# Kernel optimization log

Measured on AMD Instinct MI355X. Metric: run time of the kernel, lower is better.

## Reference

```python
import jax, jax.numpy as jnp
import numpy as np

HIDDEN = 768
ENT = 9
D = 64  # inner_dim
BIG = 1e12


def _rope_tables(seq_len, dim):
    # layout after torch stack([sin,cos],-1).reshape: [sin0,cos0,sin1,cos1,...]
    pos = jnp.arange(seq_len, dtype=jnp.float32)[:, None]          # [S,1]
    inv = jnp.power(10000.0, -2.0 * jnp.arange(dim // 2, dtype=jnp.float32) / dim)
    ang = pos * inv                                                 # [S,D/2]
    # repeat_interleave(2): [c0,c0,c1,c1,...]
    cos = jnp.repeat(jnp.cos(ang), 2, axis=-1)[:, None, :]          # [S,1,D]
    sin = jnp.repeat(jnp.sin(ang), 2, axis=-1)[:, None, :]
    return sin, cos


def _rotate_half_interleaved(x):
    # stack([-x_odd, x_even], -1).reshape -> [-x1, x0, -x3, x2, ...]
    return jnp.stack([-x[..., 1::2], x[..., ::2]], axis=-1).reshape(x.shape)


def _multilabel_ce(logits, labels):
    # standard GlobalPointer multilabel categorical crossentropy
    B = logits.shape[0]
    y_pred = logits.reshape(B * ENT, -1)
    y_true = labels.reshape(B * ENT, -1)
    y_pred = (1.0 - 2.0 * y_true) * y_pred
    y_neg = y_pred - y_true * BIG
    y_pos = y_pred - (1.0 - y_true) * BIG
    neg = jnp.logaddexp(0.0, jax.scipy.special.logsumexp(y_neg, axis=-1))
    pos = jnp.logaddexp(0.0, jax.scipy.special.logsumexp(y_pos, axis=-1))
    return jnp.mean(neg + pos)


def setup_inputs() -> dict:
    key = jax.random.key(0)
    k1, k2, k3, k4 = jax.random.split(key, 4)
    B, S = 16, 512
    last_hidden_state = jax.random.normal(k1, (B, S, HIDDEN), dtype=jnp.float32)
    attention_mask = jnp.ones((B, S), dtype=jnp.int32)
    batch_labels = jax.random.randint(k2, (B, ENT, S, S), 0, 2).astype(jnp.int32)
    W = jax.random.normal(k3, (HIDDEN, ENT * D * 2), dtype=jnp.float32) * 0.02
    b = jnp.zeros((ENT * D * 2,), dtype=jnp.float32)
    return {"last_hidden_state": last_hidden_state, "attention_mask": attention_mask,
            "batch_labels": batch_labels, "W": W, "b": b}


def reference(last_hidden_state, attention_mask, batch_labels, W, b):
    B, S, _ = last_hidden_state.shape
    out = last_hidden_state @ W + b                     # [B,S,ENT*2D]
    out = out.reshape(B, S, ENT, 2 * D)
    qw, kw = out[..., :D], out[..., D:]                 # [B,S,ENT,D]

    sin, cos = _rope_tables(S, D)                       # [S,1,D]
    qw = qw * cos + _rotate_half_interleaved(qw) * sin
    kw = kw * cos + _rotate_half_interleaved(kw) * sin

    logits = jnp.einsum('bmhd,bnhd->bhmn', qw, kw)      # [B,ENT,S,S]

    pad = attention_mask.astype(jnp.float32)[:, None, None, :]  # mask over key dim n
    logits = logits * pad - (1.0 - pad) * BIG
    tril = jnp.tril(jnp.ones((S, S), dtype=jnp.float32), -1)
    logits = logits - tril * BIG
    temp_logits = logits / (D ** 0.5)

    loss = _multilabel_ce(temp_logits, batch_labels.astype(jnp.float32))
    return loss, temp_logits
```

## Files before the change

kernel.cpp:

```cpp
#include <hip/hip_runtime.h>
#include <hip/hip_bf16.h>

#define HID 768
#define ENTS 9
#define DD 64
#define NOUT 1152
#define BATCH 16
#define SEQ 512
#define BIGF 1000000000000.0f
#define BIG8 125000000000.0f
#define NCHUNK 16

typedef __attribute__((ext_vector_type(8))) short short8;
typedef __attribute__((ext_vector_type(4))) short short4_t;
typedef __attribute__((ext_vector_type(4))) float floatx4;
typedef __attribute__((ext_vector_type(2))) float floatx2;
typedef __attribute__((ext_vector_type(4))) int intx4;
typedef unsigned short ushort_t;

static __device__ __forceinline__ ushort_t f2bf(float x) {
    unsigned int u = __float_as_uint(x);
    unsigned int r = (u + 0x7FFFu + ((u >> 16) & 1u)) >> 16;
    return (ushort_t)r;
}

static __device__ __forceinline__ void gload16(const void* g, void* l) {
    __builtin_amdgcn_global_load_lds(
        (const __attribute__((address_space(1))) void*)g,
        (__attribute__((address_space(3))) void*)l, 16, 0, 0);
}

__global__ __launch_bounds__(256) void prep_kernel(
    const float* __restrict__ X, const float* __restrict__ W,
    float* __restrict__ sin_t, float* __restrict__ cos_t,
    ushort_t* __restrict__ Xb, ushort_t* __restrict__ Wt)
{
    const int tid = blockIdx.x * 256 + threadIdx.x;
    const int nth = gridDim.x * 256;

    for (int idx = tid; idx < SEQ * 32; idx += nth) {
        int m = idx >> 5, i = idx & 31;
        float inv = powf(10000.0f, -2.0f * (float)i / 64.0f);
        float ang = (float)m * inv;
        sin_t[idx] = sinf(ang);
        cos_t[idx] = cosf(ang);
    }
    for (int idx = tid; idx < NOUT * HID; idx += nth) {
        int n = idx / HID, k = idx - n * HID;
        Wt[idx] = f2bf(W[(size_t)k * NOUT + n]);
    }
    const int nx4 = BATCH * SEQ * HID / 4;
    for (int idx = tid; idx < nx4; idx += nth) {
        float4 f = *(const float4*)&X[idx * 4];
        ushort_t* p = &Xb[idx * 4];
        p[0] = f2bf(f.x); p[1] = f2bf(f.y); p[2] = f2bf(f.z); p[3] = f2bf(f.w);
    }
}

__global__ __launch_bounds__(256) void proj_rope_kernel(
    const ushort_t* __restrict__ Xb, const ushort_t* __restrict__ Wt,
    const float* __restrict__ bias,
    const float* __restrict__ sin_t, const float* __restrict__ cos_t,
    ushort_t* __restrict__ qbuf, ushort_t* __restrict__ kbuf)
{
    __shared__ ushort_t As[128 * 32];
    __shared__ ushort_t Bs[128 * 32];
    const int tid  = threadIdx.x;
    const int lane = tid & 63;
    const int wave = tid >> 6;
    const int bm = blockIdx.x * 128;
    const int bn = blockIdx.y * 128;
    const int wm = (wave >> 1) * 64;
    const int wn = (wave & 1) * 64;

    floatx4 acc[4][4];
    #pragma unroll
    for (int j = 0; j < 4; ++j)
        #pragma unroll
        for (int i = 0; i < 4; ++i) { floatx4 z = {0.f,0.f,0.f,0.f}; acc[j][i] = z; }

    const int c0 = wave * 64 + lane;
    const int c1 = 256 + wave * 64 + lane;
    const int r0 = c0 >> 2, q0 = (c0 & 3) * 8;
    const int r1 = c1 >> 2, q1 = (c1 & 3) * 8;
    ushort_t* ldsA0 = As + wave * 512;
    ushort_t* ldsA1 = As + 2048 + wave * 512;
    ushort_t* ldsB0 = Bs + wave * 512;
    ushort_t* ldsB1 = Bs + 2048 + wave * 512;

    const int ko = (lane >> 4) * 8;
    const int lr = lane & 15;

    for (int kt = 0; kt < HID; kt += 32) {
        gload16(&Xb[(size_t)(bm + r0) * HID + kt + q0], ldsA0);
        gload16(&Xb[(size_t)(bm + r1) * HID + kt + q1], ldsA1);
        gload16(&Wt[(size_t)(bn + r0) * HID + kt + q0], ldsB0);
        gload16(&Wt[(size_t)(bn + r1) * HID + kt + q1], ldsB1);
        __syncthreads();

        short8 a[4], b[4];
        #pragma unroll
        for (int i = 0; i < 4; ++i) a[i] = *(const short8*)&As[(wm + i*16 + lr) * 32 + ko];
        #pragma unroll
        for (int j = 0; j < 4; ++j) b[j] = *(const short8*)&Bs[(wn + j*16 + lr) * 32 + ko];
        #pragma unroll
        for (int j = 0; j < 4; ++j)
            #pragma unroll
            for (int i = 0; i < 4; ++i)
                acc[j][i] = __builtin_amdgcn_mfma_f32_16x16x32_bf16(b[j], a[i], acc[j][i], 0, 0, 0);
        __syncthreads();
    }

    #pragma unroll
    for (int j = 0; j < 4; ++j) {
        const int n0 = bn + wn + j*16 + (lane >> 4) * 4;
        const int e   = n0 >> 7;
        const int dd0 = n0 & 127;
        const bool isq = dd0 < DD;
        const int d0  = isq ? dd0 : dd0 - DD;
        const float4 bv = *(const float4*)&bias[n0];
        #pragma unroll
        for (int i = 0; i < 4; ++i) {
            const int m = bm + wm + i*16 + lr;
            const int s  = m & (SEQ - 1);
            const int bb = m >> 9;
            const float c0f = cos_t[s*32 + (d0 >> 1)];
            const float s0f = sin_t[s*32 + (d0 >> 1)];
            const float c1f = cos_t[s*32 + (d0 >> 1) + 1];
            const float s1f = sin_t[s*32 + (d0 >> 1) + 1];
            const float v0 = acc[j][i][0] + bv.x;
            const float v1 = acc[j][i][1] + bv.y;
            const float v2 = acc[j][i][2] + bv.z;
            const float v3 = acc[j][i][3] + bv.w;
            const float o0 = v0 * c0f - v1 * s0f;
            const float o1 = v1 * c0f + v0 * s0f;
            const float o2 = v2 * c1f - v3 * s1f;
            const float o3 = v3 * c1f + v2 * s1f;
            short4_t sv = { (short)f2bf(o0), (short)f2bf(o1), (short)f2bf(o2), (short)f2bf(o3) };
            size_t oidx = (((size_t)(bb * ENTS + e) * SEQ) + s) * DD + d0;
            *(short4_t*)&(isq ? qbuf : kbuf)[oidx] = sv;
        }
    }
}

__global__ __launch_bounds__(256) void qk_mask_ce_kernel(
    const ushort_t* __restrict__ qbuf, const ushort_t* __restrict__ kbuf,
    const int* __restrict__ amask, const int* __restrict__ labels,
    float* __restrict__ logits, float* __restrict__ partials)
{
    __shared__ ushort_t Qs[128][72];
    __shared__ ushort_t Ks[128][72];
    __shared__ float ssn[4], ssp[4];
    const int tid  = threadIdx.x;
    const int xy = blockIdx.x;
    const int bh = blockIdx.y;
    const int bx = xy >> 2, by = xy & 3;
    const int bm = bx * 128;
    const int bn = by * 128;
    const int b  = bh / ENTS;
    const int bhbase = bh << 18;

    if (bx > by) {
        const int c4 = (tid & 31) << 2;
        const int rr = tid >> 5;

        const intx4 pf = *(const intx4*)&amask[(b << 9) + bn + c4];
        floatx4 cv;
        #pragma unroll
        for (int e = 0; e < 4; ++e) cv[e] = (float)pf[e] * BIG8 - 2.0f * BIG8;
        float cvm1 = 0.f;
        if (c4 > 0) {
            const int pfm1 = amask[(b << 9) + bn + c4 - 1];
            cvm1 = (float)pfm1 * BIG8 - 2.0f * BIG8;
        }
        const floatx4 sh = { cvm1, cv.x, cv.y, cv.z };
        const floatx2 h2 = { cv.y, cv.z };

        int cnt = 0;
        for (int pass = 0; pass < 16; ++pass) {
            const int m = bm + pass * 8 + rr;
            const int off = bhbase + (m << 9) + bn + c4;
            const intx4 y4 = __builtin_nontemporal_load((const intx4*)&labels[off]);
            #pragma unroll
            for (int e = 0; e < 4; ++e) cnt += (y4[e] & 1) & pf[e];
            if (c4 == 0) {
                logits[off] = cv.x;
                *(floatx2*)&logits[off + 1] = h2;
            } else {
                *(floatx4*)&logits[off - 1] = sh;
            }
            if (c4 == 124) logits[off + 3] = cv.w;
        }

        #pragma unroll
        for (int o = 32; o > 0; o >>= 1) cnt += __shfl_down(cnt, o);
        if ((tid & 63) == 0) ssn[tid >> 6] = (float)cnt;
        __syncthreads();
        if (tid == 0) {
            float SP = ssn[0] + ssn[1] + ssn[2] + ssn[3];
            floatx2 res = { 0.f, SP };
            *(floatx2*)&partials[(size_t)(bh * NCHUNK + xy) * 2] = res;
        }
        return;
    }

    const int lane = tid & 63;
    const int wave = tid >> 6;
    const int wm = (wave >> 1) * 64;
    const int wn = (wave & 1) * 64;
    const size_t base = (size_t)bh * SEQ * DD;

    const int g  = lane >> 4;
    const int lr = lane & 15;
    const int ko = g * 8;
    const int r0 = bm + wm + lr;
    const int W  = bn + wn;
    const int n00 = W + (g << 2);

    const bool diag = (bx == by);

    intx4 y[4][4];
    #pragma unroll
    for (int j = 0; j < 4; ++j)
        #pragma unroll
        for (int i = 0; i < 4; ++i)
            y[j][i] = __builtin_nontemporal_load(
                (const intx4*)&labels[bhbase + ((r0 + i*16) << 9) + n00 + j*16]);

    floatx4 pm8[4], pc[4];
    #pragma unroll
    for (int j = 0; j < 4; ++j) {
        const intx4 p4 = *(const intx4*)&amask[(b << 9) + n00 + j*16];
        #pragma unroll
        for (int rg = 0; rg < 4; ++rg) {
            const float pf = (float)p4[rg];
            pm8[j][rg] = pf * 0.125f;
            pc[j][rg]  = (pf - 1.0f) * BIG8;
        }
    }

    {
        const int r  = tid >> 1;
        const int ks = (tid & 1) * 32;
        const ushort_t* gq = &qbuf[base + (size_t)(bm + r) * DD + ks];
        const ushort_t* gk = &kbuf[base + (size_t)(bn + r) * DD + ks];
        #pragma unroll
        for (int uu = 0; uu < 4; ++uu) {
            *(short8*)&Qs[r][ks + uu*8] = *(const short8*)(gq + uu*8);
            *(short8*)&Ks[r][ks + uu*8] = *(const short8*)(gk + uu*8);
        }
    }
    __syncthreads();

    short8 a[2][4];
    #pragma unroll
    for (int kk = 0; kk < 2; ++kk)
        #pragma unroll
        for (int i = 0; i < 4; ++i)
            a[kk][i] = *(const short8*)&Qs[wm + i*16 + lr][kk*32 + ko];

    float smn = 0.f, smp = 0.f;
    float tl[4];
    float* __restrict__ lgb = logits + bhbase;

    #pragma unroll
    for (int jp = 0; jp < 2; ++jp) {
        const int jA = jp * 2, jB = jp * 2 + 1;

        floatx4 accA[4], accB[4];
        #pragma unroll
        for (int i = 0; i < 4; ++i) { floatx4 z = {0.f,0.f,0.f,0.f}; accA[i] = z; accB[i] = z; }
        #pragma unroll
        for (int kk = 0; kk < 2; ++kk) {
            const short8 bfA = *(const short8*)&Ks[wn + jA*16 + lr][kk*32 + ko];
            const short8 bfB = *(const short8*)&Ks[wn + jB*16 + lr][kk*32 + ko];
            #pragma unroll
            for (int i = 0; i < 4; ++i) {
                accA[i] = __builtin_amdgcn_mfma_f32_16x16x32_bf16(bfA, a[kk][i], accA[i], 0, 0, 0);
                accB[i] = __builtin_amdgcn_mfma_f32_16x16x32_bf16(bfB, a[kk][i], accB[i], 0, 0, 0);
            }
        }

        #pragma unroll
        for (int half = 0; half < 2; ++half) {
            const int j = half ? jB : jA;
            const floatx4 pm = pm8[j], pcj = pc[j];
            const int n0j = W + j*16 + (g << 2);
            #pragma unroll
            for (int i = 0; i < 4; ++i) {
                const int m = r0 + i*16;
                const int d = m - n0j;
                floatx4 v = half ? accB[i] : accA[i];
                const intx4 yv = y[j][i];
                #pragma unroll
                for (int rg = 0; rg < 4; ++rg) {
                    float t = fmaf(v[rg], pm[rg], pcj[rg]);
                    if (diag && (d > rg)) t -= BIG8;
                    v[rg] = t;
                    const int yy = yv[rg] & 1;
                    const float uu = __uint_as_float(__float_as_uint(t) ^ ((unsigned)yy << 31));
                    const float cN = yy ? -BIGF : 0.0f;
                    const float cP = yy ? -BIG8 : -BIGF;
                    smn += __expf(uu + cN);
                    smp += __expf(uu + cP);
                }
                if (half) accB[i] = v; else accA[i] = v;
            }
        }

        #pragma unroll
        for (int i = 0; i < 4; ++i) {
            const floatx4 vA = accA[i], vB = accB[i];
            const int m = r0 + i*16;
            float* __restrict__ row = lgb + (m << 9);
            const float sameA  = __shfl(vA.w, (lane - 16) & 63);
            const float tailA  = __shfl(tl[i], lr + 48);
            const float sameB  = __shfl(vB.w, (lane - 16) & 63);
            const float crossB = __shfl(vA.w, lr + 48);
            const float uA0 = (g == 0) ? tailA  : sameA;
            const float uB0 = (g == 0) ? crossB : sameB;
            if (jp == 0 && g == 0) {
                row[W] = vA.x;
                floatx2 h2 = { vA.y, vA.z };
                *(floatx2*)&row[W + 1] = h2;
            } else {
                floatx4 uA = { uA0, vA.x, vA.y, vA.z };
                *(floatx4*)&row[W + jA*16 + (g << 2) - 1] = uA;
            }
            floatx4 uB = { uB0, vB.x, vB.y, vB.z };
            *(floatx4*)&row[W + jB*16 + (g << 2) - 1] = uB;
            tl[i] = vB.w;
        }
    }

    if (g == 3) {
        #pragma unroll
        for (int i = 0; i < 4; ++i) {
            const int m = r0 + i*16;
            lgb[(m << 9) + W + 63] = tl[i];
        }
    }

    #pragma unroll
    for (int off = 32; off > 0; off >>= 1) {
        smn += __shfl_down(smn, off);
        smp += __shfl_down(smp, off);
    }
    if (lane == 0) { ssn[wave] = smn; ssp[wave] = smp; }
    __syncthreads();
    if (tid == 0) {
        float SN = ssn[0] + ssn[1] + ssn[2] + ssn[3];
        float SP = ssp[0] + ssp[1] + ssp[2] + ssp[3];
        floatx2 res = { SN, SP };
        *(floatx2*)&partials[(size_t)(bh * NCHUNK + xy) * 2] = res;
    }
}

static __device__ __forceinline__ float lae0(float x) {
    return fmaxf(x, 0.f) + log1pf(__expf(-fabsf(x)));
}

__global__ __launch_bounds__(256) void ce_final_kernel(
    const float* __restrict__ partials, float* __restrict__ out)
{
    __shared__ float red[256];
    const int t = threadIdx.x;
    float val = 0.f;
    if (t < BATCH * ENTS) {
        float SN = 0.f, SP = 0.f;
        for (int c = 0; c < NCHUNK; ++c) {
            SN += partials[(size_t)(t * NCHUNK + c) * 2];
            SP += partials[(size_t)(t * NCHUNK + c) * 2 + 1];
        }
        const float neg = log1pf(SN);
        const float pos = lae0(BIG8 + logf(SP));
        val = neg + pos;
    }
    red[t] = val;
    __syncthreads();
    for (int s2 = 128; s2 > 0; s2 >>= 1) {
        if (t < s2) red[t] += red[t + s2];
        __syncthreads();
    }
    if (t == 0) out[0] = red[0] / (float)(BATCH * ENTS);
}

extern "C" void kernel_launch(void* const* d_in, const int* in_sizes, int n_in,
                              void* d_out, int out_size, void* d_ws, size_t ws_size,
                              hipStream_t stream) {
    const float* X      = (const float*)d_in[0];
    const int*   amask  = (const int*)d_in[1];
    const int*   labels = (const int*)d_in[2];
    const float* W      = (const float*)d_in[3];
    const float* bias   = (const float*)d_in[4];

    float* out    = (float*)d_out;
    float* logits = out + 1;

    float* sin_t = (float*)d_ws;
    float* cos_t = sin_t + SEQ * 32;
    ushort_t* Xb   = (ushort_t*)(cos_t + SEQ * 32);
    ushort_t* Wt   = Xb + (size_t)BATCH * SEQ * HID;
    ushort_t* qbuf = Wt + (size_t)NOUT * HID;
    ushort_t* kbuf = qbuf + (size_t)BATCH * ENTS * SEQ * DD;
    float* partials = (float*)(kbuf + (size_t)BATCH * ENTS * SEQ * DD);

    prep_kernel<<<1024, 256, 0, stream>>>(X, W, sin_t, cos_t, Xb, Wt);
    proj_rope_kernel<<<dim3(64, 9), 256, 0, stream>>>(Xb, Wt, bias, sin_t, cos_t, qbuf, kbuf);
    qk_mask_ce_kernel<<<dim3(16, 144), 256, 0, stream>>>(qbuf, kbuf, amask, labels, logits, partials);
    ce_final_kernel<<<1, 256, 0, stream>>>(partials, out);
}
```

Baseline: 136.0 us.

## Pack labels into bitmask, load labels in halves, and remap block order across XCDs

The label tile is now loaded in two halves: the second half is fetched while the first half is consumed, and the first half is packed into a 32-bit bitmask. This cuts the registers the labels hold, which may raise occupancy or avoid spills. Blocks are launched on a 1D grid and remapped so that consecutive blocks sent to each XCD cover contiguous (batch, head) tiles, aiming at better L2 locality. Nontemporal loads on labels are replaced by normal loads, which changes cache behaviour and may pollute the cache on a stream that is read once.

```diff
diff --git a/kernel.cpp b/kernel.cpp
--- a/kernel.cpp
+++ b/kernel.cpp
@@ -152,8 +152,10 @@
     __shared__ ushort_t Ks[128][72];
     __shared__ float ssn[4], ssp[4];
     const int tid  = threadIdx.x;
-    const int xy = blockIdx.x;
-    const int bh = blockIdx.y;
+
+    const int wrk = (blockIdx.x & 7) * 288 + (blockIdx.x >> 3);
+    const int bh = wrk >> 4;
+    const int xy = wrk & 15;
     const int bx = xy >> 2, by = xy & 3;
     const int bm = bx * 128;
     const int bn = by * 128;
@@ -180,7 +182,7 @@
         for (int pass = 0; pass < 16; ++pass) {
             const int m = bm + pass * 8 + rr;
             const int off = bhbase + (m << 9) + bn + c4;
-            const intx4 y4 = __builtin_nontemporal_load((const intx4*)&labels[off]);
+            const intx4 y4 = *(const intx4*)&labels[off];
             #pragma unroll
             for (int e = 0; e < 4; ++e) cnt += (y4[e] & 1) & pf[e];
             if (c4 == 0) {
@@ -219,13 +221,12 @@
 
     const bool diag = (bx == by);
 
-    intx4 y[4][4];
-    #pragma unroll
-    for (int j = 0; j < 4; ++j)
+    intx4 yc[2][4];
+    #pragma unroll
+    for (int jh = 0; jh < 2; ++jh)
         #pragma unroll
         for (int i = 0; i < 4; ++i)
-            y[j][i] = __builtin_nontemporal_load(
-                (const intx4*)&labels[bhbase + ((r0 + i*16) << 9) + n00 + j*16]);
+            yc[jh][i] = *(const intx4*)&labels[bhbase + ((r0 + i*16) << 9) + n00 + jh*16];
 
     floatx4 pm8[4], pc[4];
     #pragma unroll
@@ -281,6 +282,29 @@
             }
         }
 
+        unsigned int yb = 0;
+        {
+            int cnt = 0;
+            #pragma unroll
+            for (int jh = 0; jh < 2; ++jh)
+                #pragma unroll
+                for (int i = 0; i < 4; ++i)
+                    #pragma unroll
+                    for (int rg = 0; rg < 4; ++rg) {
+                        yb |= (unsigned)(yc[jh][i][rg] & 1) << cnt;
+                        ++cnt;
+                    }
+        }
+
+        if (jp == 0) {
+            #pragma unroll
+            for (int jh = 0; jh < 2; ++jh)
+                #pragma unroll
+                for (int i = 0; i < 4; ++i)
+                    yc[jh][i] = *(const intx4*)&labels[bhbase + ((r0 + i*16) << 9) + n00 + (2 + jh)*16];
+        }
+
+        int cnt = 0;
         #pragma unroll
         for (int half = 0; half < 2; ++half) {
             const int j = half ? jB : jA;
@@ -291,18 +315,18 @@
                 const int m = r0 + i*16;
                 const int d = m - n0j;
                 floatx4 v = half ? accB[i] : accA[i];
-                const intx4 yv = y[j][i];
                 #pragma unroll
                 for (int rg = 0; rg < 4; ++rg) {
                     float t = fmaf(v[rg], pm[rg], pcj[rg]);
                     if (diag && (d > rg)) t -= BIG8;
                     v[rg] = t;
-                    const int yy = yv[rg] & 1;
+                    const int yy = (int)((yb >> cnt) & 1u);
                     const float uu = __uint_as_float(__float_as_uint(t) ^ ((unsigned)yy << 31));
                     const float cN = yy ? -BIGF : 0.0f;
                     const float cP = yy ? -BIG8 : -BIGF;
                     smn += __expf(uu + cN);
                     smp += __expf(uu + cP);
+                    ++cnt;
                 }
                 if (half) accB[i] = v; else accA[i] = v;
             }
@@ -407,6 +431,6 @@
 
     prep_kernel<<<1024, 256, 0, stream>>>(X, W, sin_t, cos_t, Xb, Wt);
     proj_rope_kernel<<<dim3(64, 9), 256, 0, stream>>>(Xb, Wt, bias, sin_t, cos_t, qbuf, kbuf);
-    qk_mask_ce_kernel<<<dim3(16, 144), 256, 0, stream>>>(qbuf, kbuf, amask, labels, logits, partials);
+    qk_mask_ce_kernel<<<2304, 256, 0, stream>>>(qbuf, kbuf, amask, labels, logits, partials);
     ce_final_kernel<<<1, 256, 0, stream>>>(partials, out);
 }
```

Result: no change. 134.2 us (-1.3%).
